# Kernel optimization log

Measured on AMD Instinct MI355X. Metric: run time of the kernel, lower is better.

## Reference

```python
import jax, jax.numpy as jnp
import numpy as np

NU, B, N, D = 3, 16, 1024, 256  # n_utils, batch, tokens per util, embed dim


def l2norm(x, axis=-1, eps=1e-12):
    # F.normalize over channel dim: x / max(||x||_2, eps)
    n = jnp.linalg.norm(x, axis=axis, keepdims=True)
    return x / jnp.maximum(n, eps)


def setup_inputs() -> dict:
    key = jax.random.key(0)
    ks = jax.random.split(key, 20)
    s = 0.05
    return {
        "u0": jax.random.normal(ks[0], (B, N, D), jnp.float32),
        "u1": jax.random.normal(ks[1], (B, N, D), jnp.float32),
        "u2": jax.random.normal(ks[2], (B, N, D), jnp.float32),
        # Unary per util: embed Conv1d(D,D,1), feature_reduce Conv1d(D,1,1)
        "Wu": jax.random.normal(ks[3], (NU, D, D), jnp.float32) * s,
        "bu": jax.random.normal(ks[4], (NU, D), jnp.float32) * s,
        "wr": jax.random.normal(ks[5], (NU, D), jnp.float32) * s,
        "br": jax.random.normal(ks[6], (NU,), jnp.float32) * s,
        # Self Pairwise per util: embed_X, embed_Y Conv1d(D,D,1)
        "Wsx": jax.random.normal(ks[7], (NU, D, D), jnp.float32) * s,
        "bsx": jax.random.normal(ks[8], (NU, D), jnp.float32) * s,
        "Wsy": jax.random.normal(ks[9], (NU, D, D), jnp.float32) * s,
        "bsy": jax.random.normal(ks[10], (NU, D), jnp.float32) * s,
        # Cross Pairwise per ordered pair (i,j), i!=j (diagonal unused)
        "Wpx": jax.random.normal(ks[11], (NU, NU, D, D), jnp.float32) * s,
        "bpx": jax.random.normal(ks[12], (NU, NU, D), jnp.float32) * s,
        "Wpy": jax.random.normal(ks[13], (NU, NU, D, D), jnp.float32) * s,
        "bpy": jax.random.normal(ks[14], (NU, NU, D), jnp.float32) * s,
        # reduce_potentials: (i,i) -> Conv1d(4,1,1,bias=False); (i,j) -> Conv1d(3,1,1,bias=False)
        "wdiag": jax.random.normal(ks[15], (NU, 4), jnp.float32) * s,
        "wpair": jax.random.normal(ks[16], (NU, NU, 3), jnp.float32) * s,
    }


def _forward(u0, u1, u2, Wu, bu, wr, br, Wsx, bsx, Wsy, bsy,
             Wpx, bpx, Wpy, bpy, wdiag, wpair):
    U = jnp.stack([u0, u1, u2])  # (NU, b, n, d)

    # --- Unary potentials (eval mode: dropout = identity) ---
    Xe = jnp.einsum('ubnd,ued->ubne', U, Wu) + bu[:, None, None, :]
    unary = jnp.einsum('ubne,ue->ubn', jax.nn.relu(Xe), wr) + br[:, None, None]  # (NU,b,n)

    # --- Self Pairwise (x_spatial_dim=None path): embed, cosine-normalize over channels, affinity, mean ---
    Xs = l2norm(jnp.einsum('ubnd,ued->ubne', U, Wsx) + bsx[:, None, None, :])
    Ys = l2norm(jnp.einsum('ubnd,ued->ubne', U, Wsy) + bsy[:, None, None, :])
    S_self = jnp.einsum('ubne,ubme->ubnm', Xs, Ys)  # (NU,b,n,n)
    self_pot = S_self.mean(axis=3)                   # X_poten only (Y is None)  (NU,b,n)

    # --- Cross Pairwise over all ordered pairs (u,v) ---
    Xp = l2norm(jnp.einsum('ubnd,uved->uvbne', U, Wpx) + bpx[:, :, None, None, :])
    Yp = l2norm(jnp.einsum('vbnd,uved->uvbne', U, Wpy) + bpy[:, :, None, None, :])
    S = jnp.einsum('uvbne,uvbme->uvbnm', Xp, Yp)     # (NU,NU,b,n,n)
    pot_x = S.mean(axis=4)  # poten for util u in pair (u,v): (NU,NU,b,n)
    pot_y = S.mean(axis=3)  # poten for util v in pair (u,v): (NU,NU,b,n)

    # --- Reduce potentials per (target i, source j), softmax-attend over source tokens ---
    rows = []
    for i in range(NU):
        row = []
        for j in range(NU):
            if i == j:
                pots = [unary[i], self_pot[i]] + [pot_x[i, k] for k in range(NU) if k != i]
                w = wdiag[i]            # (4,)
            else:
                pots = [unary[j], self_pot[j], pot_y[i, j]]
                w = wpair[i, j]         # (3,)
            P = jnp.stack(pots, axis=1)                 # (b, k, n)
            red = jnp.einsum('bkn,k->bn', P, w)         # Conv1d(k,1,1,bias=False)
            a = jax.nn.softmax(red, axis=1)             # (b, n)
            row.append(jnp.einsum('bnd,bn->bd', U[j], a))  # attended feature (b, d)
        rows.append(jnp.stack(row))
    return jnp.stack(rows)  # (NU, NU, b, d)


def reference(u0, u1, u2, Wu, bu, wr, br, Wsx, bsx, Wsy, bsy,
              Wpx, bpx, Wpy, bpy, wdiag, wpair):
    return _forward(u0, u1, u2, Wu, bu, wr, br, Wsx, bsx, Wsy, bsy,
                    Wpx, bpx, Wpy, bpy, wdiag, wpair)
```

## Files before the change

kernel.cpp:

```cpp
#include <hip/hip_runtime.h>
#include <math.h>

#define NU 3
#define BB 16
#define NN 1024
#define DD 256
#define MM (BB*NN)
#define NPAIR 6

#define OFF_UNARY  0
#define OFF_INVXS  (OFF_UNARY + NU*MM)
#define OFF_INVXP  (OFF_INVXS + NU*MM)
#define OFF_INVYP  (OFF_INVXP + NPAIR*MM)
#define OFF_YBAR   (OFF_INVYP + NPAIR*MM)
#define OFF_XPBAR  (OFF_YBAR + NU*BB*DD)
#define OFF_YPBAR  (OFF_XPBAR + NPAIR*BB*DD)
#define OFF_PROJS  (OFF_YPBAR + NPAIR*BB*DD)
#define OFF_PROJX  (OFF_PROJS + NU*BB*DD)
#define OFF_PROJY  (OFF_PROJX + NPAIR*BB*DD)
#define OFF_CSS    (OFF_PROJY + NPAIR*BB*DD)
#define OFF_CSX    (OFF_CSS + NU*BB)
#define OFF_CSY    (OFF_CSX + NPAIR*BB)
#define OFF_SELFP  (OFF_CSY + NPAIR*BB)
#define OFF_POTX   (OFF_SELFP + NU*MM)
#define OFF_POTY   (OFF_POTX + NPAIR*MM)
#define WS_FLOATS  (OFF_POTY + NPAIR*MM)
#define OFF_PROB   (WS_FLOATS + 21*32768)
#define OFF_PART   (OFF_PROB + 9*BB*NN)

typedef _Float16 half8 __attribute__((ext_vector_type(8)));
typedef float f32x4 __attribute__((ext_vector_type(4)));

__device__ __forceinline__ const float* selU(int u, const float* u0, const float* u1, const float* u2) {
    return u == 0 ? u0 : (u == 1 ? u1 : u2);
}
__device__ __forceinline__ half8 cvt8(float4 a, float4 b) {
    half8 h = { (_Float16)a.x,(_Float16)a.y,(_Float16)a.z,(_Float16)a.w,
                (_Float16)b.x,(_Float16)b.y,(_Float16)b.z,(_Float16)b.w };
    return h;
}

__global__ __launch_bounds__(256) void convw_kernel(
    const float* __restrict__ Wu, const float* __restrict__ Wsx, const float* __restrict__ Wsy,
    const float* __restrict__ Wpx, const float* __restrict__ Wpy, float* __restrict__ ws)
{
    const int slot = blockIdx.x;
    const int kc   = blockIdx.y;
    const int tid  = threadIdx.x;
    const int u = slot / 7, s = slot % 7;
    const int j0 = (u==0)?1:0, j1 = (u==2)?1:2;
    const float* W =
        s==0 ? Wu  + (size_t)u*DD*DD :
        s==1 ? Wsx + (size_t)u*DD*DD :
        s==2 ? Wsy + (size_t)u*DD*DD :
        s==3 ? Wpx + (size_t)(u*NU+j0)*DD*DD :
        s==4 ? Wpx + (size_t)(u*NU+j1)*DD*DD :
        s==5 ? Wpy + (size_t)(j0*NU+u)*DD*DD :
               Wpy + (size_t)(j1*NU+u)*DD*DD;
    _Float16* wh = (_Float16*)(ws + WS_FLOATS) + (size_t)slot*65536;
    #pragma unroll
    for (int g = 0; g < 4; ++g) {
        const int idx16 = g*256 + tid;
        const int et   = idx16 >> 6;
        const int lane = idx16 & 63;
        const int e  = et*16 + (lane & 15);
        const int k0 = kc*32 + (lane >> 4)*8;
        const float* sp = W + (size_t)e*DD + k0;
        const float4 v0 = *reinterpret_cast<const float4*>(sp);
        const float4 v1 = *reinterpret_cast<const float4*>(sp + 4);
        *reinterpret_cast<half8*>(wh + ((size_t)(et*8 + kc)*64 + lane)*8) = cvt8(v0, v1);
    }
}

__global__ __launch_bounds__(256, 2) void pass1_kernel(
    const float* __restrict__ u0, const float* __restrict__ u1, const float* __restrict__ u2,
    const float* __restrict__ bu, const float* __restrict__ wr, const float* __restrict__ br,
    const float* __restrict__ bsx, const float* __restrict__ bsy,
    const float* __restrict__ bpx, const float* __restrict__ bpy,
    float* __restrict__ ws)
{
    __shared__ __align__(16) _Float16 Ub[16384];
    __shared__ float ep_sum[4][64];
    __shared__ float ep_inv[64];

    const int tid  = threadIdx.x;
    const int u    = blockIdx.y;
    const int row0 = blockIdx.x * 64;
    const int b    = row0 >> 10;

    const int j0 = (u==0)?1:0, j1 = (u==2)?1:2;
    const int px0 = u*2, px1 = u*2+1;
    const int py0 = (u==0)?2:((u==1)?0:1);
    const int py1 = (u==0)?4:((u==1)?5:3);

    const float* src = selU(u,u0,u1,u2);
    const _Float16* whU = (const _Float16*)(ws + WS_FLOATS) + (size_t)u*7*65536;

    const int lane = tid & 63, wq = tid >> 6;
    const int l15 = lane & 15, lg = lane >> 4;
    const int swz = (l15 >> 1) & 3;
    const int kxor = (lg ^ swz) * 8;

    const _Float16* wbase = whU + (size_t)wq*16384 + (size_t)lane*8;

    f32x4 acc[4][4];
    #pragma unroll
    for (int m = 0; m < 4; ++m)
        #pragma unroll
        for (int n = 0; n < 4; ++n) acc[m][n] = (f32x4)0.f;

    half8 bfA[4], bfB[4];
    half8 af[4][8];

#define BFLD(DST, S, KC) { \
    _Pragma("unroll") \
    for (int n_ = 0; n_ < 4; ++n_) \
        DST[n_] = *reinterpret_cast<const half8*>(wbase + (size_t)(S)*65536 + n_*4096 + (KC)*512); }

#define MFMAS(KC, BF) { \
    _Pragma("unroll") \
    for (int n_ = 0; n_ < 4; ++n_) { \
        _Pragma("unroll") \
        for (int m_ = 0; m_ < 4; ++m_) \
            acc[m_][n_] = __builtin_amdgcn_mfma_f32_16x16x32_f16(af[m_][KC], BF[n_], acc[m_][n_],0,0,0); } }

#define SLAB(KC, BFC, BFN) { \
    if ((KC) < 7) { BFLD(BFN, s, (KC)+1) } else if (s < 6) { BFLD(BFN, s+1, 0) } \
    MFMAS(KC, BFC) }

    BFLD(bfA, 0, 0)

    #pragma unroll
    for (int c = 0; c < 8; ++c) {
        const int G2 = c*256 + tid;
        const int t  = G2 >> 5;
        const int gk = G2 & 31;
        const int kc = gk >> 2, kg = gk & 3;
        const float* p = src + (size_t)(row0 + t)*DD + gk*8;
        const float4 v0 = *reinterpret_cast<const float4*>(p);
        const float4 v1 = *reinterpret_cast<const float4*>(p + 4);
        const int kgs = kg ^ ((t >> 1) & 3);
        *reinterpret_cast<half8*>(&Ub[kc*2048 + t*32 + kgs*8]) = cvt8(v0, v1);
    }
    __syncthreads();

    #pragma unroll
    for (int kc = 0; kc < 8; ++kc) {
        #pragma unroll
        for (int m = 0; m < 4; ++m)
            af[m][kc] = *reinterpret_cast<const half8*>(&Ub[kc*2048 + (m*16 + l15)*32 + kxor]);
    }

    for (int s = 0; s < 7; ++s) {
        SLAB(0, bfA, bfB)
        SLAB(1, bfB, bfA)
        SLAB(2, bfA, bfB)
        SLAB(3, bfB, bfA)
        SLAB(4, bfA, bfB)
        SLAB(5, bfB, bfA)
        SLAB(6, bfA, bfB)
        SLAB(7, bfB, bfA)

        const float* bias =
            s==0 ? bu  + u*DD :
            s==1 ? bsx + u*DD :
            s==2 ? bsy + u*DD :
            s==3 ? bpx + (u*NU+j0)*DD :
            s==4 ? bpx + (u*NU+j1)*DD :
            s==5 ? bpy + (j0*NU+u)*DD :
                   bpy + (j1*NU+u)*DD;
        float bv[4];
        #pragma unroll
        for (int n = 0; n < 4; ++n) bv[n] = bias[wq*64 + n*16 + l15];
        #pragma unroll
        for (int m = 0; m < 4; ++m)
            #pragma unroll
            for (int n = 0; n < 4; ++n)
                #pragma unroll
                for (int r = 0; r < 4; ++r) acc[m][n][r] += bv[n];

        if (s == 0) {
            float wrv[4];
            #pragma unroll
            for (int n = 0; n < 4; ++n) wrv[n] = wr[u*DD + wq*64 + n*16 + l15];
            float pm[4][4];
            #pragma unroll
            for (int m = 0; m < 4; ++m)
                #pragma unroll
                for (int r = 0; r < 4; ++r) {
                    float t = 0.f;
                    #pragma unroll
                    for (int n = 0; n < 4; ++n) t = fmaf(fmaxf(acc[m][n][r], 0.f), wrv[n], t);
                    pm[m][r] = t;
                }
            #pragma unroll
            for (int mask = 1; mask <= 8; mask <<= 1)
                #pragma unroll
                for (int m = 0; m < 4; ++m)
                    #pragma unroll
                    for (int r = 0; r < 4; ++r) pm[m][r] += __shfl_xor(pm[m][r], mask);
            if (l15 == 0) {
                #pragma unroll
                for (int m = 0; m < 4; ++m)
                    #pragma unroll
                    for (int r = 0; r < 4; ++r) ep_sum[wq][m*16 + lg*4 + r] = pm[m][r];
            }
            __syncthreads();
            if (tid < 64)
                ws[OFF_UNARY + (size_t)u*MM + row0 + tid] =
                    ep_sum[0][tid]+ep_sum[1][tid]+ep_sum[2][tid]+ep_sum[3][tid] + br[u];
        } else {
            float pm[4][4];
            #pragma unroll
            for (int m = 0; m < 4; ++m)
                #pragma unroll
                for (int r = 0; r < 4; ++r) {
                    float t = 0.f;
                    #pragma unroll
                    for (int n = 0; n < 4; ++n) t = fmaf(acc[m][n][r], acc[m][n][r], t);
                    pm[m][r] = t;
                }
            #pragma unroll
            for (int mask = 1; mask <= 8; mask <<= 1)
                #pragma unroll
                for (int m = 0; m < 4; ++m)
                    #pragma unroll
                    for (int r = 0; r < 4; ++r) pm[m][r] += __shfl_xor(pm[m][r], mask);
            if (l15 == 0) {
                #pragma unroll
                for (int m = 0; m < 4; ++m)
                    #pragma unroll
                    for (int r = 0; r < 4; ++r) ep_sum[wq][m*16 + lg*4 + r] = pm[m][r];
            }
            __syncthreads();
            if (tid < 64) {
                const float ssum = ep_sum[0][tid]+ep_sum[1][tid]+ep_sum[2][tid]+ep_sum[3][tid];
                const float inv = 1.f / fmaxf(sqrtf(ssum), 1e-12f);
                ep_inv[tid] = inv;
                if (s == 1)      ws[OFF_INVXS + (size_t)u  *MM + row0 + tid] = inv;
                else if (s == 3) ws[OFF_INVXP + (size_t)px0*MM + row0 + tid] = inv;
                else if (s == 4) ws[OFF_INVXP + (size_t)px1*MM + row0 + tid] = inv;
                else if (s == 5) ws[OFF_INVYP + (size_t)py0*MM + row0 + tid] = inv;
                else if (s == 6) ws[OFF_INVYP + (size_t)py1*MM + row0 + tid] = inv;
            }
            __syncthreads();
            if (s >= 2) {
                float invv[4][4];
                #pragma unroll
                for (int m = 0; m < 4; ++m)
                    #pragma unroll
                    for (int r = 0; r < 4; ++r) invv[m][r] = ep_inv[m*16 + lg*4 + r];
                float qn[4];
                #pragma unroll
                for (int n = 0; n < 4; ++n) {
                    float t = 0.f;
                    #pragma unroll
                    for (int m = 0; m < 4; ++m)
                        #pragma unroll
                        for (int r = 0; r < 4; ++r) t = fmaf(acc[m][n][r], invv[m][r], t);
                    qn[n] = t;
                }
                #pragma unroll
                for (int n = 0; n < 4; ++n) {
                    qn[n] += __shfl_xor(qn[n], 16);
                    qn[n] += __shfl_xor(qn[n], 32);
                }
                float* bar =
                    s==2 ? ws + OFF_YBAR  + ((size_t)u  *BB + b)*DD :
                    s==3 ? ws + OFF_XPBAR + ((size_t)px0*BB + b)*DD :
                    s==4 ? ws + OFF_XPBAR + ((size_t)px1*BB + b)*DD :
                    s==5 ? ws + OFF_YPBAR + ((size_t)py0*BB + b)*DD :
                           ws + OFF_YPBAR + ((size_t)py1*BB + b)*DD;
                if (lane < 16) {
                    #pragma unroll
                    for (int n = 0; n < 4; ++n)
                        atomicAdd(&bar[wq*64 + n*16 + lane], qn[n]);
                }
            }
        }
        #pragma unroll
        for (int m = 0; m < 4; ++m)
            #pragma unroll
            for (int n = 0; n < 4; ++n) acc[m][n] = (f32x4)0.f;
        __syncthreads();
    }
#undef BFLD
#undef MFMAS
#undef SLAB
}

__global__ __launch_bounds__(256) void proj_kernel(
    const float* __restrict__ Wsx, const float* __restrict__ bsx,
    const float* __restrict__ Wpx, const float* __restrict__ bpx,
    const float* __restrict__ Wpy, const float* __restrict__ bpy,
    float* __restrict__ ws)
{
    __shared__ float barl[DD];
    __shared__ float redl[256];
    const int task = blockIdx.x >> 4;
    const int b    = blockIdx.x & 15;
    const int tid  = threadIdx.x;
    const float *W, *bias, *barp;
    float *projp, *csp;
    if (task < 3) {
        const int uu = task;
        W = Wsx + (size_t)uu*DD*DD; bias = bsx + uu*DD;
        barp  = ws + OFF_YBAR  + ((size_t)uu*BB + b)*DD;
        projp = ws + OFF_PROJS + ((size_t)uu*BB + b)*DD;
        csp   = ws + OFF_CSS + uu*BB + b;
    } else if (task < 9) {
        const int p = task - 3; const int i = p>>1;
        const int j = (p&1) == 0 ? (i==0?1:0) : (i==2?1:2);
        W = Wpx + (size_t)(i*NU+j)*DD*DD; bias = bpx + (i*NU+j)*DD;
        barp  = ws + OFF_YPBAR + ((size_t)p*BB + b)*DD;
        projp = ws + OFF_PROJX + ((size_t)p*BB + b)*DD;
        csp   = ws + OFF_CSX + p*BB + b;
    } else {
        const int p = task - 9; const int i = p>>1;
        const int j = (p&1) == 0 ? (i==0?1:0) : (i==2?1:2);
        W = Wpy + (size_t)(i*NU+j)*DD*DD; bias = bpy + (i*NU+j)*DD;
        barp  = ws + OFF_XPBAR + ((size_t)p*BB + b)*DD;
        projp = ws + OFF_PROJY + ((size_t)p*BB + b)*DD;
        csp   = ws + OFF_CSY + p*BB + b;
    }
    barl[tid] = barp[tid] * (1.f / NN);
    __syncthreads();
    float s = 0.f;
    for (int e = 0; e < DD; ++e) s = fmaf(W[(size_t)e*DD + tid], barl[e], s);
    projp[tid] = s;
    redl[tid] = bias[tid] * barl[tid];
    __syncthreads();
    for (int st = 128; st > 0; st >>= 1) {
        if (tid < st) redl[tid] += redl[tid + st];
        __syncthreads();
    }
    if (tid == 0) *csp = redl[0];
}

__global__ __launch_bounds__(256) void pots_kernel(
    const float* __restrict__ u0, const float* __restrict__ u1, const float* __restrict__ u2,
    float* __restrict__ ws)
{
    __shared__ float projl[5][DD];
    __shared__ float csl[5];
    const int u    = blockIdx.y;
    const int row0 = blockIdx.x * 32;
    const int b    = row0 >> 10;
    const int tid  = threadIdx.x;
    const int px0 = u*2, px1 = u*2+1;
    const int py0 = (u==0)?2:((u==1)?0:1);
    const int py1 = (u==0)?4:((u==1)?5:3);

    projl[0][tid] = ws[OFF_PROJS + ((size_t)u  *BB + b)*DD + tid];
    projl[1][tid] = ws[OFF_PROJX + ((size_t)px0*BB + b)*DD + tid];
    projl[2][tid] = ws[OFF_PROJX + ((size_t)px1*BB + b)*DD + tid];
    projl[3][tid] = ws[OFF_PROJY + ((size_t)py0*BB + b)*DD + tid];
    projl[4][tid] = ws[OFF_PROJY + ((size_t)py1*BB + b)*DD + tid];
    if (tid == 0) {
        csl[0] = ws[OFF_CSS + u*BB + b];
        csl[1] = ws[OFF_CSX + px0*BB + b];
        csl[2] = ws[OFF_CSX + px1*BB + b];
        csl[3] = ws[OFF_CSY + py0*BB + b];
        csl[4] = ws[OFF_CSY + py1*BB + b];
    }
    __syncthreads();
    const float* src = selU(u,u0,u1,u2);
    const int token = tid >> 3, q = tid & 7;
    const int row = row0 + token;
    float a0=0.f,a1=0.f,a2=0.f,a3=0.f,a4=0.f;
    #pragma unroll
    for (int cc = 0; cc < 8; ++cc) {
        const int d0 = q*32 + cc*4;
        const float4 v  = *reinterpret_cast<const float4*>(src + (size_t)row*DD + d0);
        const float4 p0 = *reinterpret_cast<const float4*>(&projl[0][d0]);
        const float4 p1 = *reinterpret_cast<const float4*>(&projl[1][d0]);
        const float4 p2 = *reinterpret_cast<const float4*>(&projl[2][d0]);
        const float4 p3 = *reinterpret_cast<const float4*>(&projl[3][d0]);
        const float4 p4 = *reinterpret_cast<const float4*>(&projl[4][d0]);
        a0 = fmaf(v.x,p0.x,fmaf(v.y,p0.y,fmaf(v.z,p0.z,fmaf(v.w,p0.w,a0))));
        a1 = fmaf(v.x,p1.x,fmaf(v.y,p1.y,fmaf(v.z,p1.z,fmaf(v.w,p1.w,a1))));
        a2 = fmaf(v.x,p2.x,fmaf(v.y,p2.y,fmaf(v.z,p2.z,fmaf(v.w,p2.w,a2))));
        a3 = fmaf(v.x,p3.x,fmaf(v.y,p3.y,fmaf(v.z,p3.z,fmaf(v.w,p3.w,a3))));
        a4 = fmaf(v.x,p4.x,fmaf(v.y,p4.y,fmaf(v.z,p4.z,fmaf(v.w,p4.w,a4))));
    }
    #pragma unroll
    for (int mask = 1; mask <= 4; mask <<= 1) {
        a0 += __shfl_xor(a0, mask, 8);
        a1 += __shfl_xor(a1, mask, 8);
        a2 += __shfl_xor(a2, mask, 8);
        a3 += __shfl_xor(a3, mask, 8);
        a4 += __shfl_xor(a4, mask, 8);
    }
    if (q == 0) {
        ws[OFF_SELFP + (size_t)u  *MM + row] = (a0 + csl[0]) * ws[OFF_INVXS + (size_t)u  *MM + row];
        ws[OFF_POTX  + (size_t)px0*MM + row] = (a1 + csl[1]) * ws[OFF_INVXP + (size_t)px0*MM + row];
        ws[OFF_POTX  + (size_t)px1*MM + row] = (a2 + csl[2]) * ws[OFF_INVXP + (size_t)px1*MM + row];
        ws[OFF_POTY  + (size_t)py0*MM + row] = (a3 + csl[3]) * ws[OFF_INVYP + (size_t)py0*MM + row];
        ws[OFF_POTY  + (size_t)py1*MM + row] = (a4 + csl[4]) * ws[OFF_INVYP + (size_t)py1*MM + row];
    }
}

__global__ __launch_bounds__(256) void attend_logits_kernel(
    const float* __restrict__ wdiag, const float* __restrict__ wpair,
    float* __restrict__ ws)
{
    __shared__ float el[3][NN];
    __shared__ float redl[256];
    const int c = blockIdx.x;
    const int j = c >> 4, b = c & 15;
    const int tid = threadIdx.x;

    #pragma unroll
    for (int i = 0; i < 3; ++i) {
        if (i == j) {
            const int p1 = i*2, p2 = i*2+1;
            const float w0 = wdiag[i*4+0], w1 = wdiag[i*4+1], w2 = wdiag[i*4+2], w3 = wdiag[i*4+3];
            for (int n = tid; n < NN; n += 256) {
                const int row = b*NN + n;
                el[i][n] = w0*ws[OFF_UNARY + i*MM + row] + w1*ws[OFF_SELFP + i*MM + row]
                         + w2*ws[OFF_POTX + p1*MM + row] + w3*ws[OFF_POTX + p2*MM + row];
            }
        } else {
            const int p = i*2 + (j > i ? j-1 : j);
            const float w0 = wpair[(i*3+j)*3+0], w1 = wpair[(i*3+j)*3+1], w2 = wpair[(i*3+j)*3+2];
            for (int n = tid; n < NN; n += 256) {
                const int row = b*NN + n;
                el[i][n] = w0*ws[OFF_UNARY + j*MM + row] + w1*ws[OFF_SELFP + j*MM + row]
                         + w2*ws[OFF_POTY + p*MM + row];
            }
        }
    }
    __syncthreads();
    #pragma unroll
    for (int i = 0; i < 3; ++i) {
        float m = -1e30f;
        for (int n = tid; n < NN; n += 256) m = fmaxf(m, el[i][n]);
        redl[tid] = m; __syncthreads();
        for (int st = 128; st > 0; st >>= 1) {
            if (tid < st) redl[tid] = fmaxf(redl[tid], redl[tid+st]);
            __syncthreads();
        }
        m = redl[0];
        __syncthreads();
        float ss = 0.f;
        for (int n = tid; n < NN; n += 256) {
            const float e = expf(el[i][n] - m);
            el[i][n] = e;
            ss += e;
        }
        redl[tid] = ss; __syncthreads();
        for (int st = 128; st > 0; st >>= 1) {
            if (tid < st) redl[tid] += redl[tid+st];
            __syncthreads();
        }
        const float invS = 1.f / redl[0];
        __syncthreads();
        for (int n = tid; n < NN; n += 256)
            ws[OFF_PROB + ((size_t)(i*3+j)*BB + b)*NN + n] = el[i][n] * invS;
    }
}

__global__ __launch_bounds__(256) void attend_sum_kernel(
    const float* __restrict__ u0, const float* __restrict__ u1, const float* __restrict__ u2,
    const float* __restrict__ ws, float* __restrict__ wso)
{
    __shared__ float pl[3][128];
    const int x  = blockIdx.x;
    const int jb = x >> 3, ch = x & 7;
    const int j = jb >> 4, b = jb & 15;
    const int tid = threadIdx.x;

    for (int t = tid; t < 384; t += 256) {
        const int i = t >> 7, n = t & 127;
        pl[i][n] = ws[OFF_PROB + ((size_t)(i*3+j)*BB + b)*NN + ch*128 + n];
    }
    __syncthreads();
    const float* Uj = selU(j, u0, u1, u2) + ((size_t)b*NN + ch*128)*DD;
    float a0 = 0.f, a1 = 0.f, a2 = 0.f;
    #pragma unroll 4
    for (int n = 0; n < 128; ++n) {
        const float v = Uj[(size_t)n*DD + tid];
        a0 = fmaf(pl[0][n], v, a0);
        a1 = fmaf(pl[1][n], v, a1);
        a2 = fmaf(pl[2][n], v, a2);
    }
    wso[OFF_PART + (((size_t)(0*3+j)*BB + b)*8 + ch)*DD + tid] = a0;
    wso[OFF_PART + (((size_t)(1*3+j)*BB + b)*8 + ch)*DD + tid] = a1;
    wso[OFF_PART + (((size_t)(2*3+j)*BB + b)*8 + ch)*DD + tid] = a2;
}

__global__ __launch_bounds__(256) void attend_reduce_kernel(
    const float* __restrict__ ws, float* __restrict__ out)
{
    const int ijb = blockIdx.x;
    const int tid = threadIdx.x;
    float s = 0.f;
    #pragma unroll
    for (int ch = 0; ch < 8; ++ch)
        s += ws[OFF_PART + ((size_t)ijb*8 + ch)*DD + tid];
    out[(size_t)ijb*DD + tid] = s;
}

extern "C" void kernel_launch(void* const* d_in, const int* in_sizes, int n_in,
                              void* d_out, int out_size, void* d_ws, size_t ws_size,
                              hipStream_t stream)
{
    (void)in_sizes; (void)n_in; (void)out_size; (void)ws_size;
    const float* u0    = (const float*)d_in[0];
    const float* u1    = (const float*)d_in[1];
    const float* u2    = (const float*)d_in[2];
    const float* Wu    = (const float*)d_in[3];
    const float* bu    = (const float*)d_in[4];
    const float* wr    = (const float*)d_in[5];
    const float* br    = (const float*)d_in[6];
    const float* Wsx   = (const float*)d_in[7];
    const float* bsx   = (const float*)d_in[8];
    const float* Wsy   = (const float*)d_in[9];
    const float* bsy   = (const float*)d_in[10];
    const float* Wpx   = (const float*)d_in[11];
    const float* bpx   = (const float*)d_in[12];
    const float* Wpy   = (const float*)d_in[13];
    const float* bpy   = (const float*)d_in[14];
    const float* wdiag = (const float*)d_in[15];
    const float* wpair = (const float*)d_in[16];
    float* ws  = (float*)d_ws;
    float* out = (float*)d_out;

    hipMemsetAsync(ws + OFF_YBAR, 0, (size_t)(NU + 2*NPAIR)*BB*DD*sizeof(float), stream);

    dim3 gw(21, 8);
    convw_kernel<<<gw, 256, 0, stream>>>(Wu, Wsx, Wsy, Wpx, Wpy, ws);

    dim3 g1(MM/64, 3);
    pass1_kernel<<<g1, 256, 0, stream>>>(u0,u1,u2,bu,wr,br,bsx,bsy,bpx,bpy,ws);

    proj_kernel<<<15*BB, 256, 0, stream>>>(Wsx,bsx,Wpx,bpx,Wpy,bpy,ws);
    dim3 g2(MM/32, 3);
    pots_kernel<<<g2, 256, 0, stream>>>(u0,u1,u2,ws);

    attend_logits_kernel<<<3*BB, 256, 0, stream>>>(wdiag, wpair, ws);
    attend_sum_kernel<<<3*BB*8, 256, 0, stream>>>(u0,u1,u2, ws, ws);
    attend_reduce_kernel<<<9*BB, 256, 0, stream>>>(ws, out);
}
```

Baseline: 157.0 us.

## Double pass1 row tile to 128 rows, reload A fragments from LDS per k-slab

The pass1 GEMM block now covers 128 token rows instead of 64. Each wave's weight (B) fragments are therefore reused across twice as many MFMAs, which halves global weight traffic per output row. A fragments are no longer kept in registers for all k-slabs; they are reloaded from LDS for each slab, so the larger accumulator tile fits in registers. The trade-offs are more LDS use (64KB of fp16 staging), more LDS reads, and a grid half as large, which may reduce occupancy and block-level parallelism.

```diff
diff --git a/kernel.cpp b/kernel.cpp
--- a/kernel.cpp
+++ b/kernel.cpp
@@ -79,13 +79,13 @@
     const float* __restrict__ bpx, const float* __restrict__ bpy,
     float* __restrict__ ws)
 {
-    __shared__ __align__(16) _Float16 Ub[16384];
-    __shared__ float ep_sum[4][64];
-    __shared__ float ep_inv[64];
+    __shared__ __align__(16) _Float16 Ub[32768];
+    __shared__ float ep_sum[4][128];
+    __shared__ float ep_inv[128];
 
     const int tid  = threadIdx.x;
     const int u    = blockIdx.y;
-    const int row0 = blockIdx.x * 64;
+    const int row0 = blockIdx.x * 128;
     const int b    = row0 >> 10;
 
     const int j0 = (u==0)?1:0, j1 = (u==2)?1:2;
@@ -103,35 +103,35 @@
 
     const _Float16* wbase = whU + (size_t)wq*16384 + (size_t)lane*8;
 
-    f32x4 acc[4][4];
-    #pragma unroll
-    for (int m = 0; m < 4; ++m)
+    f32x4 acc[8][4];
+    #pragma unroll
+    for (int m = 0; m < 8; ++m)
         #pragma unroll
         for (int n = 0; n < 4; ++n) acc[m][n] = (f32x4)0.f;
 
     half8 bfA[4], bfB[4];
-    half8 af[4][8];
 
 #define BFLD(DST, S, KC) { \
     _Pragma("unroll") \
     for (int n_ = 0; n_ < 4; ++n_) \
         DST[n_] = *reinterpret_cast<const half8*>(wbase + (size_t)(S)*65536 + n_*4096 + (KC)*512); }
 
-#define MFMAS(KC, BF) { \
-    _Pragma("unroll") \
-    for (int n_ = 0; n_ < 4; ++n_) { \
-        _Pragma("unroll") \
-        for (int m_ = 0; m_ < 4; ++m_) \
-            acc[m_][n_] = __builtin_amdgcn_mfma_f32_16x16x32_f16(af[m_][KC], BF[n_], acc[m_][n_],0,0,0); } }
-
 #define SLAB(KC, BFC, BFN) { \
     if ((KC) < 7) { BFLD(BFN, s, (KC)+1) } else if (s < 6) { BFLD(BFN, s+1, 0) } \
-    MFMAS(KC, BFC) }
+    half8 afd[8]; \
+    _Pragma("unroll") \
+    for (int m_ = 0; m_ < 8; ++m_) \
+        afd[m_] = *reinterpret_cast<const half8*>(&Ub[(KC)*4096 + (m_*16 + l15)*32 + kxor]); \
+    _Pragma("unroll") \
+    for (int n_ = 0; n_ < 4; ++n_) \
+        _Pragma("unroll") \
+        for (int m_ = 0; m_ < 8; ++m_) \
+            acc[m_][n_] = __builtin_amdgcn_mfma_f32_16x16x32_f16(afd[m_], BFC[n_], acc[m_][n_],0,0,0); }
 
     BFLD(bfA, 0, 0)
 
     #pragma unroll
-    for (int c = 0; c < 8; ++c) {
+    for (int c = 0; c < 16; ++c) {
         const int G2 = c*256 + tid;
         const int t  = G2 >> 5;
         const int gk = G2 & 31;
@@ -140,16 +140,9 @@
         const float4 v0 = *reinterpret_cast<const float4*>(p);
         const float4 v1 = *reinterpret_cast<const float4*>(p + 4);
         const int kgs = kg ^ ((t >> 1) & 3);
-        *reinterpret_cast<half8*>(&Ub[kc*2048 + t*32 + kgs*8]) = cvt8(v0, v1);
+        *reinterpret_cast<half8*>(&Ub[kc*4096 + t*32 + kgs*8]) = cvt8(v0, v1);
     }
     __syncthreads();
-
-    #pragma unroll
-    for (int kc = 0; kc < 8; ++kc) {
-        #pragma unroll
-        for (int m = 0; m < 4; ++m)
-            af[m][kc] = *reinterpret_cast<const half8*>(&Ub[kc*2048 + (m*16 + l15)*32 + kxor]);
-    }
 
     for (int s = 0; s < 7; ++s) {
         SLAB(0, bfA, bfB)
@@ -173,7 +166,7 @@
         #pragma unroll
         for (int n = 0; n < 4; ++n) bv[n] = bias[wq*64 + n*16 + l15];
         #pragma unroll
-        for (int m = 0; m < 4; ++m)
+        for (int m = 0; m < 8; ++m)
             #pragma unroll
             for (int n = 0; n < 4; ++n)
                 #pragma unroll
@@ -183,9 +176,9 @@
             float wrv[4];
             #pragma unroll
             for (int n = 0; n < 4; ++n) wrv[n] = wr[u*DD + wq*64 + n*16 + l15];
-            float pm[4][4];
-            #pragma unroll
-            for (int m = 0; m < 4; ++m)
+            float pm[8][4];
+            #pragma unroll
+            for (int m = 0; m < 8; ++m)
                 #pragma unroll
                 for (int r = 0; r < 4; ++r) {
                     float t = 0.f;
@@ -196,23 +189,23 @@
             #pragma unroll
             for (int mask = 1; mask <= 8; mask <<= 1)
                 #pragma unroll
-                for (int m = 0; m < 4; ++m)
+                for (int m = 0; m < 8; ++m)
                     #pragma unroll
                     for (int r = 0; r < 4; ++r) pm[m][r] += __shfl_xor(pm[m][r], mask);
             if (l15 == 0) {
                 #pragma unroll
-                for (int m = 0; m < 4; ++m)
+                for (int m = 0; m < 8; ++m)
                     #pragma unroll
                     for (int r = 0; r < 4; ++r) ep_sum[wq][m*16 + lg*4 + r] = pm[m][r];
             }
             __syncthreads();
-            if (tid < 64)
+            if (tid < 128)
                 ws[OFF_UNARY + (size_t)u*MM + row0 + tid] =
                     ep_sum[0][tid]+ep_sum[1][tid]+ep_sum[2][tid]+ep_sum[3][tid] + br[u];
         } else {
-            float pm[4][4];
-            #pragma unroll
-            for (int m = 0; m < 4; ++m)
+            float pm[8][4];
+            #pragma unroll
+            for (int m = 0; m < 8; ++m)
                 #pragma unroll
                 for (int r = 0; r < 4; ++r) {
                     float t = 0.f;
@@ -223,17 +216,17 @@
             #pragma unroll
             for (int mask = 1; mask <= 8; mask <<= 1)
                 #pragma unroll
-                for (int m = 0; m < 4; ++m)
+                for (int m = 0; m < 8; ++m)
                     #pragma unroll
                     for (int r = 0; r < 4; ++r) pm[m][r] += __shfl_xor(pm[m][r], mask);
             if (l15 == 0) {
                 #pragma unroll
-                for (int m = 0; m < 4; ++m)
+                for (int m = 0; m < 8; ++m)
                     #pragma unroll
                     for (int r = 0; r < 4; ++r) ep_sum[wq][m*16 + lg*4 + r] = pm[m][r];
             }
             __syncthreads();
-            if (tid < 64) {
+            if (tid < 128) {
                 const float ssum = ep_sum[0][tid]+ep_sum[1][tid]+ep_sum[2][tid]+ep_sum[3][tid];
                 const float inv = 1.f / fmaxf(sqrtf(ssum), 1e-12f);
                 ep_inv[tid] = inv;
@@ -245,20 +238,18 @@
             }
             __syncthreads();
             if (s >= 2) {
-                float invv[4][4];
-                #pragma unroll
-                for (int m = 0; m < 4; ++m)
-                    #pragma unroll
-                    for (int r = 0; r < 4; ++r) invv[m][r] = ep_inv[m*16 + lg*4 + r];
                 float qn[4];
                 #pragma unroll
-                for (int n = 0; n < 4; ++n) {
-                    float t = 0.f;
-                    #pragma unroll
-                    for (int m = 0; m < 4; ++m)
+                for (int n = 0; n < 4; ++n) qn[n] = 0.f;
+                #pragma unroll
+                for (int m = 0; m < 8; ++m) {
+                    float invv[4];
+                    #pragma unroll
+                    for (int r = 0; r < 4; ++r) invv[r] = ep_inv[m*16 + lg*4 + r];
+                    #pragma unroll
+                    for (int n = 0; n < 4; ++n)
                         #pragma unroll
-                        for (int r = 0; r < 4; ++r) t = fmaf(acc[m][n][r], invv[m][r], t);
-                    qn[n] = t;
+                        for (int r = 0; r < 4; ++r) qn[n] = fmaf(acc[m][n][r], invv[r], qn[n]);
                 }
                 #pragma unroll
                 for (int n = 0; n < 4; ++n) {
@@ -279,13 +270,12 @@
             }
         }
         #pragma unroll
-        for (int m = 0; m < 4; ++m)
+        for (int m = 0; m < 8; ++m)
             #pragma unroll
             for (int n = 0; n < 4; ++n) acc[m][n] = (f32x4)0.f;
         __syncthreads();
     }
 #undef BFLD
-#undef MFMAS
 #undef SLAB
 }
 
@@ -531,7 +521,7 @@
     dim3 gw(21, 8);
     convw_kernel<<<gw, 256, 0, stream>>>(Wu, Wsx, Wsy, Wpx, Wpy, ws);
 
-    dim3 g1(MM/64, 3);
+    dim3 g1(MM/128, 3);
     pass1_kernel<<<g1, 256, 0, stream>>>(u0,u1,u2,bu,wr,br,bsx,bsy,bpx,bpy,ws);
 
     proj_kernel<<<15*BB, 256, 0, stream>>>(Wsx,bsx,Wpx,bpx,Wpy,bpy,ws);
```

Measured after the change: 131.5 us. -16.3%, faster.

## Stage fp16 weight slabs into LDS via async global_load_lds double buffering

Applied to the files above, without the earlier changes.

Weight tiles for the pass1 GEMM were loaded directly from global memory into registers, and all A fragments were preloaded into registers. Now each k-chunk of weights is copied into a double-buffered LDS area with global_load_lds, the convw layout is changed to match, and A fragments are read from LDS per k-chunk. The goal is lower register pressure and asynchronous weight prefetch. The cost is a __syncthreads after every k-chunk (56 per block) and extra LDS traffic, which could hurt occupancy or stall the MFMA pipeline.

```diff
diff --git a/kernel.cpp b/kernel.cpp
--- a/kernel.cpp
+++ b/kernel.cpp
@@ -39,6 +39,12 @@
                 (_Float16)b.x,(_Float16)b.y,(_Float16)b.z,(_Float16)b.w };
     return h;
 }
+__device__ __forceinline__ void gload16(const _Float16* g, _Float16* l) {
+    __builtin_amdgcn_global_load_lds(
+        (const __attribute__((address_space(1))) void*)g,
+        (__attribute__((address_space(3))) void*)l,
+        16, 0, 0);
+}
 
 __global__ __launch_bounds__(256) void convw_kernel(
     const float* __restrict__ Wu, const float* __restrict__ Wsx, const float* __restrict__ Wsy,
@@ -57,18 +63,17 @@
         s==4 ? Wpx + (size_t)(u*NU+j1)*DD*DD :
         s==5 ? Wpy + (size_t)(j0*NU+u)*DD*DD :
                Wpy + (size_t)(j1*NU+u)*DD*DD;
-    _Float16* wh = (_Float16*)(ws + WS_FLOATS) + (size_t)slot*65536;
+    _Float16* wh = (_Float16*)(ws + WS_FLOATS) + (size_t)slot*65536 + (size_t)kc*8192;
     #pragma unroll
     for (int g = 0; g < 4; ++g) {
         const int idx16 = g*256 + tid;
-        const int et   = idx16 >> 6;
         const int lane = idx16 & 63;
-        const int e  = et*16 + (lane & 15);
+        const int e  = (idx16 >> 6)*16 + (lane & 15);
         const int k0 = kc*32 + (lane >> 4)*8;
         const float* sp = W + (size_t)e*DD + k0;
         const float4 v0 = *reinterpret_cast<const float4*>(sp);
         const float4 v1 = *reinterpret_cast<const float4*>(sp + 4);
-        *reinterpret_cast<half8*>(wh + ((size_t)(et*8 + kc)*64 + lane)*8) = cvt8(v0, v1);
+        *reinterpret_cast<half8*>(wh + (size_t)idx16*8) = cvt8(v0, v1);
     }
 }
 
@@ -80,6 +85,7 @@
     float* __restrict__ ws)
 {
     __shared__ __align__(16) _Float16 Ub[16384];
+    __shared__ __align__(16) _Float16 Wb[2][8192];
     __shared__ float ep_sum[4][64];
     __shared__ float ep_inv[64];
 
@@ -101,34 +107,20 @@
     const int swz = (l15 >> 1) & 3;
     const int kxor = (lg ^ swz) * 8;
 
-    const _Float16* wbase = whU + (size_t)wq*16384 + (size_t)lane*8;
-
     f32x4 acc[4][4];
     #pragma unroll
     for (int m = 0; m < 4; ++m)
         #pragma unroll
         for (int n = 0; n < 4; ++n) acc[m][n] = (f32x4)0.f;
 
-    half8 bfA[4], bfB[4];
-    half8 af[4][8];
-
-#define BFLD(DST, S, KC) { \
+#define STAGE(T, BUF) { \
+    const _Float16* gsb = whU + (size_t)((T) >> 3)*65536 + (size_t)((T) & 7)*8192 \
+                        + (size_t)(wq*4)*512 + (size_t)lane*8; \
     _Pragma("unroll") \
-    for (int n_ = 0; n_ < 4; ++n_) \
-        DST[n_] = *reinterpret_cast<const half8*>(wbase + (size_t)(S)*65536 + n_*4096 + (KC)*512); }
-
-#define MFMAS(KC, BF) { \
-    _Pragma("unroll") \
-    for (int n_ = 0; n_ < 4; ++n_) { \
-        _Pragma("unroll") \
-        for (int m_ = 0; m_ < 4; ++m_) \
-            acc[m_][n_] = __builtin_amdgcn_mfma_f32_16x16x32_f16(af[m_][KC], BF[n_], acc[m_][n_],0,0,0); } }
-
-#define SLAB(KC, BFC, BFN) { \
-    if ((KC) < 7) { BFLD(BFN, s, (KC)+1) } else if (s < 6) { BFLD(BFN, s+1, 0) } \
-    MFMAS(KC, BFC) }
-
-    BFLD(bfA, 0, 0)
+    for (int i_ = 0; i_ < 4; ++i_) \
+        gload16(gsb + i_*512, &Wb[BUF][(wq*4 + i_)*512]); }
+
+    STAGE(0, 0)
 
     #pragma unroll
     for (int c = 0; c < 8; ++c) {
@@ -144,22 +136,26 @@
     }
     __syncthreads();
 
-    #pragma unroll
-    for (int kc = 0; kc < 8; ++kc) {
+    for (int s = 0; s < 7; ++s) {
         #pragma unroll
-        for (int m = 0; m < 4; ++m)
-            af[m][kc] = *reinterpret_cast<const half8*>(&Ub[kc*2048 + (m*16 + l15)*32 + kxor]);
-    }
-
-    for (int s = 0; s < 7; ++s) {
-        SLAB(0, bfA, bfB)
-        SLAB(1, bfB, bfA)
-        SLAB(2, bfA, bfB)
-        SLAB(3, bfB, bfA)
-        SLAB(4, bfA, bfB)
-        SLAB(5, bfB, bfA)
-        SLAB(6, bfA, bfB)
-        SLAB(7, bfB, bfA)
+        for (int kc = 0; kc < 8; ++kc) {
+            const int t = s*8 + kc;
+            const int cur = t & 1;
+            if (t < 55) STAGE(t+1, cur^1)
+            half8 af0 = *reinterpret_cast<const half8*>(&Ub[kc*2048 + (     l15)*32 + kxor]);
+            half8 af1 = *reinterpret_cast<const half8*>(&Ub[kc*2048 + (16 + l15)*32 + kxor]);
+            half8 af2 = *reinterpret_cast<const half8*>(&Ub[kc*2048 + (32 + l15)*32 + kxor]);
+            half8 af3 = *reinterpret_cast<const half8*>(&Ub[kc*2048 + (48 + l15)*32 + kxor]);
+            #pragma unroll
+            for (int n = 0; n < 4; ++n) {
+                const half8 bf = *reinterpret_cast<const half8*>(&Wb[cur][(wq*4 + n)*512 + lane*8]);
+                acc[0][n] = __builtin_amdgcn_mfma_f32_16x16x32_f16(af0, bf, acc[0][n],0,0,0);
+                acc[1][n] = __builtin_amdgcn_mfma_f32_16x16x32_f16(af1, bf, acc[1][n],0,0,0);
+                acc[2][n] = __builtin_amdgcn_mfma_f32_16x16x32_f16(af2, bf, acc[2][n],0,0,0);
+                acc[3][n] = __builtin_amdgcn_mfma_f32_16x16x32_f16(af3, bf, acc[3][n],0,0,0);
+            }
+            __syncthreads();
+        }
 
         const float* bias =
             s==0 ? bu  + u*DD :
@@ -284,9 +280,7 @@
             for (int n = 0; n < 4; ++n) acc[m][n] = (f32x4)0.f;
         __syncthreads();
     }
-#undef BFLD
-#undef MFMAS
-#undef SLAB
+#undef STAGE
 }
 
 __global__ __launch_bounds__(256) void proj_kernel(
```

New measurement: 154.5 us. No clear change (-1.6%).
